# Kernel optimization log

Measured on AMD Instinct MI355X. Metric: run time of the kernel, lower is better.

The kernel has to match this reference:

```python
import jax, jax.numpy as jnp
import numpy as np

# hetero-graph meta: (relation, src_type, dst_type)
RELS = [("a2b", "a", "b"), ("b2a", "b", "a"), ("a2g", "a", "g"), ("g2a", "g", "a"),
        ("b2g", "b", "g"), ("g2b", "g", "b"), ("a2a", "a", "a"), ("b2b", "b", "b"), ("g2g", "g", "g")]
N = {"a": 100000, "b": 150000, "g": 2000}
E = {"a2b": 300000, "b2a": 300000, "a2g": 100000, "g2a": 100000,
     "b2g": 150000, "g2b": 150000, "a2a": 100000, "b2b": 150000, "g2g": 2000}
D = 128
N_LAYERS = 2
BN_EPS = 1e-5


def setup_inputs() -> dict:
    key = jax.random.key(0)
    ks = jax.random.split(key, 32)
    inp = {
        "feat_a": jax.random.normal(ks[0], (N["a"], D), jnp.float32),
        "feat_b": jax.random.normal(ks[1], (N["b"], D), jnp.float32),
        "feat_g": jax.random.normal(ks[2], (N["g"], D), jnp.float32),
        "W": jax.random.normal(ks[3], (N_LAYERS, 9, D, D), jnp.float32) * (1.0 / np.sqrt(D)),
        "bias": jnp.zeros((N_LAYERS, 9, D), jnp.float32),
        "gamma": jnp.ones((N_LAYERS, 9, D), jnp.float32),
        "beta": jnp.zeros((N_LAYERS, 9, D), jnp.float32),
    }
    i = 4
    for name, st, dt in RELS:
        inp[f"e_{name}_src"] = jax.random.randint(ks[i], (E[name],), 0, N[st], jnp.int32); i += 1
        inp[f"e_{name}_dst"] = jax.random.randint(ks[i], (E[name],), 0, N[dt], jnp.int32); i += 1
    return inp


def _gconv(x_src, src, dst, n_src, n_dst, W_r, b_r, g_r, be_r):
    """DGL GraphConv(norm='both') + (eval dropout = identity) + BatchNorm1d (batch stats)."""
    ones_e = jnp.ones(src.shape[0], x_src.dtype)
    out_deg = jax.ops.segment_sum(ones_e, src, num_segments=n_src)   # src out-degree
    in_deg = jax.ops.segment_sum(ones_e, dst, num_segments=n_dst)    # dst in-degree
    ns = jnp.where(out_deg > 0, jax.lax.rsqrt(jnp.maximum(out_deg, 1.0)), 0.0)
    nd = jnp.where(in_deg > 0, jax.lax.rsqrt(jnp.maximum(in_deg, 1.0)), 0.0)
    h = x_src * ns[:, None]                                           # [n_src, D]
    m = jax.ops.segment_sum(h[src], dst, num_segments=n_dst)         # gather-scatter over edges
    out = (m @ W_r) * nd[:, None] + b_r                               # [n_dst, D]
    mu = out.mean(axis=0)
    var = out.var(axis=0)                                             # biased var, as torch BN
    return (out - mu) * jax.lax.rsqrt(var + BN_EPS) * g_r + be_r


def _forward(feat_a, feat_b, feat_g, W, bias, gamma, beta, edges):
    feat = {"a": feat_a, "b": feat_b, "g": feat_g}
    resid = feat
    for l in range(N_LAYERS):
        acc = {"a": 0.0, "b": 0.0, "g": 0.0}
        for r, (name, st, dt) in enumerate(RELS):
            src, dst = edges[name]
            acc[dt] = acc[dt] + _gconv(feat[st], src, dst, N[st], N[dt],
                                       W[l, r], bias[l, r], gamma[l, r], beta[l, r])
        feat = acc  # HeteroGraphConv aggregate='sum'
    return (feat["a"] + resid["a"], feat["b"] + resid["b"], feat["g"] + resid["g"])


def reference(feat_a, feat_b, feat_g, W, bias, gamma, beta,
              e_a2b_src, e_a2b_dst, e_b2a_src, e_b2a_dst, e_a2g_src, e_a2g_dst,
              e_g2a_src, e_g2a_dst, e_b2g_src, e_b2g_dst, e_g2b_src, e_g2b_dst,
              e_a2a_src, e_a2a_dst, e_b2b_src, e_b2b_dst, e_g2g_src, e_g2g_dst):
    edges = {"a2b": (e_a2b_src, e_a2b_dst), "b2a": (e_b2a_src, e_b2a_dst),
             "a2g": (e_a2g_src, e_a2g_dst), "g2a": (e_g2a_src, e_g2a_dst),
             "b2g": (e_b2g_src, e_b2g_dst), "g2b": (e_g2b_src, e_g2b_dst),
             "a2a": (e_a2a_src, e_a2a_dst), "b2b": (e_b2b_src, e_b2b_dst),
             "g2g": (e_g2g_src, e_g2g_dst)}
    return _forward(feat_a, feat_b, feat_g, W, bias, gamma, beta, edges)
```

## Files before the change

kernel.cpp:

```cpp
#include <hip/hip_runtime.h>
#include <cstdint>

#define D 128

typedef __attribute__((ext_vector_type(8))) short short8;
typedef __attribute__((ext_vector_type(4))) float f32x4;

__device__ inline ushort f2bf(float f) {
    uint u = __float_as_uint(f);
    uint r = (u + 0x7fffu + ((u >> 16) & 1u)) >> 16;
    return (ushort)r;
}
__device__ inline float bf2f(ushort u) { return __uint_as_float(((uint)u) << 16); }


__global__ void k_count(const int* __restrict__ src, const int* __restrict__ dst,
                        int E, float* __restrict__ degs, float* __restrict__ degd) {
    int i = blockIdx.x * blockDim.x + threadIdx.x;
    if (i < E) {
        atomicAdd(&degs[src[i]], 1.0f);
        atomicAdd(&degd[dst[i]], 1.0f);
    }
}

__global__ void k_rsqrt(float* __restrict__ p, int n) {
    int i = blockIdx.x * blockDim.x + threadIdx.x;
    if (i < n) {
        float d = p[i];
        p[i] = d > 0.0f ? rsqrtf(d) : 0.0f;
    }
}

__global__ void k_scan1(const float* __restrict__ cnt, int* __restrict__ off,
                        int* __restrict__ bsum, int n) {
    __shared__ int s[256];
    int t = threadIdx.x, i = blockIdx.x * 256 + t;
    int v = (i < n) ? (int)cnt[i] : 0;
    int acc = v;
    s[t] = acc; __syncthreads();
    for (int d = 1; d < 256; d <<= 1) {
        int add = (t >= d) ? s[t - d] : 0;
        __syncthreads();
        acc += add; s[t] = acc; __syncthreads();
    }
    if (i < n) off[i] = acc - v;
    if (t == 255) bsum[blockIdx.x] = acc;
}

__global__ __launch_bounds__(1024) void k_scan2(int* __restrict__ bsum, int nb) {
    __shared__ int s[1024];
    int t = threadIdx.x;
    int i0 = t * 3;
    int v0 = (i0     < nb) ? bsum[i0]     : 0;
    int v1 = (i0 + 1 < nb) ? bsum[i0 + 1] : 0;
    int v2 = (i0 + 2 < nb) ? bsum[i0 + 2] : 0;
    int tot = v0 + v1 + v2;
    int acc = tot;
    s[t] = acc; __syncthreads();
    for (int d = 1; d < 1024; d <<= 1) {
        int add = (t >= d) ? s[t - d] : 0;
        __syncthreads();
        acc += add; s[t] = acc; __syncthreads();
    }
    int base = acc - tot;
    if (i0     < nb) bsum[i0]     = base;
    if (i0 + 1 < nb) bsum[i0 + 1] = base + v0;
    if (i0 + 2 < nb) bsum[i0 + 2] = base + v0 + v1;
}

__global__ void k_scan3(int* __restrict__ off, const int* __restrict__ bsum, int n) {
    int i = blockIdx.x * 256 + threadIdx.x;
    if (i < n) off[i] += bsum[blockIdx.x];
}

__global__ void k_fill(const int* __restrict__ src, const int* __restrict__ dst,
                       int E, int* __restrict__ offs, int* __restrict__ sorted) {
    int e = blockIdx.x * blockDim.x + threadIdx.x;
    if (e < E) {
        int pos = atomicAdd(&offs[dst[e]], 1);
        sorted[pos] = src[e];
    }
}

__global__ void k_prepw(const float* __restrict__ W, ushort* __restrict__ Wf) {
    int i = blockIdx.x * 256 + threadIdx.x;
    if (i < 18 * 16384) {
        int r = i >> 14, j = i & 16383;
        int e = j & 7, lane = (j >> 3) & 63, kbi = (j >> 9) & 3, c = j >> 11;
        int lm = lane & 15, lg = lane >> 4;
        int k = kbi * 32 + lg * 8 + e, ncol = c * 16 + lm;
        Wf[i] = f2bf(W[(r << 14) + (k << 7) + ncol]);
    }
}


__device__ inline float4 loadx(const float* x, size_t idx) { return *(const float4*)(x + idx); }
__device__ inline float4 loadx(const ushort* x, size_t idx) {
    ushort4 u = *(const ushort4*)(x + idx);
    float4 v;
    v.x = bf2f(u.x); v.y = bf2f(u.y); v.z = bf2f(u.z); v.w = bf2f(u.w);
    return v;
}

template <typename XT>
__global__ __launch_bounds__(256) void k_gather_row(
    const XT* __restrict__ x, const float* __restrict__ ns,
    const float* __restrict__ nd,
    const int* __restrict__ OFFS, int gdbase,
    const int* __restrict__ sorted, int n_dst,
    ushort* __restrict__ m) {
    __shared__ float4 part[8][32];
    int row = blockIdx.x;
    if (row >= n_dst) return;
    int t = threadIdx.x;
    int g = t >> 5, q = t & 31;
    int c4 = q * 4;
    int gd = gdbase + row;
    int beg = (gd == 0) ? 0 : OFFS[gd - 1];
    int end = OFFS[gd];
    float4 acc = {0.f, 0.f, 0.f, 0.f};
    for (int j = beg + g; j < end; j += 8) {
        int s = sorted[j];
        float w = ns[s];
        float4 v = loadx(x, ((size_t)s << 7) + c4);
        acc.x += v.x * w; acc.y += v.y * w; acc.z += v.z * w; acc.w += v.w * w;
    }
    part[g][q] = acc;
    __syncthreads();
    if (g == 0) {
        float4 a = part[0][q];
        #pragma unroll
        for (int gg = 1; gg < 8; ++gg) {
            float4 b = part[gg][q];
            a.x += b.x; a.y += b.y; a.z += b.z; a.w += b.w;
        }
        float sc = nd[row];
        ushort4 o;
        o.x = f2bf(a.x * sc); o.y = f2bf(a.y * sc);
        o.z = f2bf(a.z * sc); o.w = f2bf(a.w * sc);
        *(ushort4*)(m + ((size_t)row << 7) + c4) = o;
    }
}

__global__ __launch_bounds__(256) void k_gemm_mfma(
    const ushort* __restrict__ mb, const ushort* __restrict__ Wf,
    int n, float* __restrict__ outp, float* __restrict__ stats) {
    __shared__ ushort Wl[16384];
    __shared__ float Sl[256];
    int t = threadIdx.x;
    int w = t >> 6, lane = t & 63, lm = lane & 15, lg = lane >> 4;
    Sl[t] = 0.0f;

    #pragma unroll
    for (int i = 0; i < 8; ++i) {
        int ci = t + 256 * i;
        *(short8*)&Wl[ci * 8] = *(const short8*)&Wf[ci * 8];
    }
    __syncthreads();

    int R = (blockIdx.x * 4 + w) * 32;
    float rs1[8] = {0.f, 0.f, 0.f, 0.f, 0.f, 0.f, 0.f, 0.f};
    float rs2[8] = {0.f, 0.f, 0.f, 0.f, 0.f, 0.f, 0.f, 0.f};

    if (R < n) {
        f32x4 acc[2][8] = {};
        int r0 = R + lm, r1 = R + 16 + lm;
        const ushort* a0p = mb + (((size_t)r0) << 7) + lg * 8;
        const ushort* a1p = mb + (((size_t)r1) << 7) + lg * 8;
        bool v0 = r0 < n, v1 = r1 < n;
        #pragma unroll
        for (int kbi = 0; kbi < 4; ++kbi) {
            short8 a0 = {}, a1 = {};
            if (v0) a0 = *(const short8*)(a0p + kbi * 32);
            if (v1) a1 = *(const short8*)(a1p + kbi * 32);
            #pragma unroll
            for (int c = 0; c < 8; ++c) {
                short8 b = *(short8*)&Wl[((c * 4 + kbi) * 64 + lane) * 8];
                acc[0][c] = __builtin_amdgcn_mfma_f32_16x16x32_bf16(a0, b, acc[0][c], 0, 0, 0);
                acc[1][c] = __builtin_amdgcn_mfma_f32_16x16x32_bf16(a1, b, acc[1][c], 0, 0, 0);
            }
        }
        #pragma unroll
        for (int m = 0; m < 2; ++m) {
            int rowb = R + m * 16 + lg * 4;
            #pragma unroll
            for (int c = 0; c < 8; ++c) {
                f32x4 v = acc[m][c];
                rs1[c] += v[0] + v[1] + v[2] + v[3];
                rs2[c] += v[0] * v[0] + v[1] * v[1] + v[2] * v[2] + v[3] * v[3];
                #pragma unroll
                for (int i2 = 0; i2 < 4; ++i2) {
                    int row = rowb + i2;
                    if (row < n)
                        outp[((size_t)row << 7) + c * 16 + lm] = v[i2];
                }
            }
        }
    }

    #pragma unroll
    for (int c = 0; c < 8; ++c) {
        float s1 = rs1[c], s2 = rs2[c];
        s1 += __shfl_xor(s1, 16); s1 += __shfl_xor(s1, 32);
        s2 += __shfl_xor(s2, 16); s2 += __shfl_xor(s2, 32);
        if (lg == 0) {
            atomicAdd(&Sl[c * 16 + lm], s1);
            atomicAdd(&Sl[128 + c * 16 + lm], s2);
        }
    }
    __syncthreads();
    atomicAdd(&stats[t], Sl[t]);
}


template <typename XT>
__global__ __launch_bounds__(512) void k_fused2(
    const XT* __restrict__ x, const float* __restrict__ ns,
    const float* __restrict__ nd,
    const int* __restrict__ OFFS, int gdbase,
    const int* __restrict__ sorted,
    const ushort* __restrict__ Wf,
    int n, float* __restrict__ outp, float* __restrict__ stats) {
    __shared__ ushort Wl[16384];
    __shared__ float Sl[256];
    int t = threadIdx.x;
    if (t < 256) Sl[t] = 0.0f;

    #pragma unroll
    for (int i = 0; i < 4; ++i) {
        int ci = t + 512 * i;
        *(short8*)&Wl[ci * 8] = *(const short8*)&Wf[ci * 8];
    }

    int w = t >> 6, lane = t & 63, lm = lane & 15, lg = lane >> 4;
    int R = blockIdx.x * 128 + w * 16;
    int row = R + lm;

    float a[4][8] = {};
    float scale = 0.0f;
    if (row < n) {
        int gd = gdbase + row;
        int beg = (gd == 0) ? 0 : OFFS[gd - 1];
        int end = OFFS[gd];
        for (int j = beg; j < end; ++j) {
            int s = sorted[j];
            float wgt = ns[s];
            size_t xb = (size_t)s << 7;
            #pragma unroll
            for (int kbi = 0; kbi < 4; ++kbi) {
                int cb = (kbi * 4 + lg) * 8;
                float4 u0 = loadx(x, xb + cb);
                float4 u1 = loadx(x, xb + cb + 4);
                a[kbi][0] += u0.x * wgt; a[kbi][1] += u0.y * wgt;
                a[kbi][2] += u0.z * wgt; a[kbi][3] += u0.w * wgt;
                a[kbi][4] += u1.x * wgt; a[kbi][5] += u1.y * wgt;
                a[kbi][6] += u1.z * wgt; a[kbi][7] += u1.w * wgt;
            }
        }
        scale = nd[row];
    }

    short8 af[4];
    #pragma unroll
    for (int kbi = 0; kbi < 4; ++kbi) {
        #pragma unroll
        for (int e = 0; e < 8; ++e)
            af[kbi][e] = (short)f2bf(a[kbi][e] * scale);
    }

    __syncthreads();

    float rs1[8] = {0.f, 0.f, 0.f, 0.f, 0.f, 0.f, 0.f, 0.f};
    float rs2[8] = {0.f, 0.f, 0.f, 0.f, 0.f, 0.f, 0.f, 0.f};

    if (R < n) {
        f32x4 acc[8] = {};
        #pragma unroll
        for (int kbi = 0; kbi < 4; ++kbi) {
            #pragma unroll
            for (int c = 0; c < 8; ++c) {
                short8 b = *(short8*)&Wl[((c * 4 + kbi) * 64 + lane) * 8];
                acc[c] = __builtin_amdgcn_mfma_f32_16x16x32_bf16(af[kbi], b, acc[c], 0, 0, 0);
            }
        }
        int rowb = R + lg * 4;
        #pragma unroll
        for (int c = 0; c < 8; ++c) {
            f32x4 v = acc[c];
            rs1[c] += v[0] + v[1] + v[2] + v[3];
            rs2[c] += v[0] * v[0] + v[1] * v[1] + v[2] * v[2] + v[3] * v[3];
            #pragma unroll
            for (int i2 = 0; i2 < 4; ++i2) {
                int crow = rowb + i2;
                if (crow < n)
                    outp[((size_t)crow << 7) + c * 16 + lm] = v[i2];
            }
        }
    }

    #pragma unroll
    for (int c = 0; c < 8; ++c) {
        float s1 = rs1[c], s2 = rs2[c];
        s1 += __shfl_xor(s1, 16); s1 += __shfl_xor(s1, 32);
        s2 += __shfl_xor(s2, 16); s2 += __shfl_xor(s2, 32);
        if (lg == 0) {
            atomicAdd(&Sl[c * 16 + lm], s1);
            atomicAdd(&Sl[128 + c * 16 + lm], s2);
        }
    }
    __syncthreads();
    if (t < 256) atomicAdd(&stats[t], Sl[t]);
}


__global__ void k_norm3_bf(const float4* __restrict__ o0, const float4* __restrict__ o1,
                           const float4* __restrict__ o2,
                           const float* __restrict__ st0, const float* __restrict__ st1,
                           const float* __restrict__ st2,
                           const float* __restrict__ g0, const float* __restrict__ g1,
                           const float* __restrict__ g2,
                           const float* __restrict__ b0, const float* __restrict__ b1,
                           const float* __restrict__ b2,
                           float inv_n, int total4, ushort* __restrict__ dst) {
    __shared__ float sc[3][128], sh[3][128];
    int t = threadIdx.x;
    if (t < 128) {
        float mu0 = st0[t] * inv_n, va0 = st0[128 + t] * inv_n - mu0 * mu0;
        float s0 = g0[t] * rsqrtf(va0 + 1e-5f); sc[0][t] = s0; sh[0][t] = b0[t] - mu0 * s0;
        float mu1 = st1[t] * inv_n, va1 = st1[128 + t] * inv_n - mu1 * mu1;
        float s1 = g1[t] * rsqrtf(va1 + 1e-5f); sc[1][t] = s1; sh[1][t] = b1[t] - mu1 * s1;
        float mu2 = st2[t] * inv_n, va2 = st2[128 + t] * inv_n - mu2 * mu2;
        float s2 = g2[t] * rsqrtf(va2 + 1e-5f); sc[2][t] = s2; sh[2][t] = b2[t] - mu2 * s2;
    }
    __syncthreads();
    for (int i = blockIdx.x * blockDim.x + t; i < total4; i += gridDim.x * blockDim.x) {
        int c4 = (i & 31) * 4;
        float4 v0 = o0[i], v1 = o1[i], v2 = o2[i];
        float4 r;
        r.x = (v0.x * sc[0][c4+0] + sh[0][c4+0]) + (v1.x * sc[1][c4+0] + sh[1][c4+0]) + (v2.x * sc[2][c4+0] + sh[2][c4+0]);
        r.y = (v0.y * sc[0][c4+1] + sh[0][c4+1]) + (v1.y * sc[1][c4+1] + sh[1][c4+1]) + (v2.y * sc[2][c4+1] + sh[2][c4+1]);
        r.z = (v0.z * sc[0][c4+2] + sh[0][c4+2]) + (v1.z * sc[1][c4+2] + sh[1][c4+2]) + (v2.z * sc[2][c4+2] + sh[2][c4+2]);
        r.w = (v0.w * sc[0][c4+3] + sh[0][c4+3]) + (v1.w * sc[1][c4+3] + sh[1][c4+3]) + (v2.w * sc[2][c4+3] + sh[2][c4+3]);
        ushort4 o;
        o.x = f2bf(r.x); o.y = f2bf(r.y); o.z = f2bf(r.z); o.w = f2bf(r.w);
        *(ushort4*)(dst + (size_t)i * 4) = o;
    }
}

__global__ void k_norm3_f32(const float4* __restrict__ o0, const float4* __restrict__ o1,
                            const float4* __restrict__ o2,
                            const float* __restrict__ st0, const float* __restrict__ st1,
                            const float* __restrict__ st2,
                            const float* __restrict__ g0, const float* __restrict__ g1,
                            const float* __restrict__ g2,
                            const float* __restrict__ b0, const float* __restrict__ b1,
                            const float* __restrict__ b2,
                            float inv_n, int total4, float4* __restrict__ dst,
                            const float4* __restrict__ resid4) {
    __shared__ float sc[3][128], sh[3][128];
    int t = threadIdx.x;
    if (t < 128) {
        float mu0 = st0[t] * inv_n, va0 = st0[128 + t] * inv_n - mu0 * mu0;
        float s0 = g0[t] * rsqrtf(va0 + 1e-5f); sc[0][t] = s0; sh[0][t] = b0[t] - mu0 * s0;
        float mu1 = st1[t] * inv_n, va1 = st1[128 + t] * inv_n - mu1 * mu1;
        float s1 = g1[t] * rsqrtf(va1 + 1e-5f); sc[1][t] = s1; sh[1][t] = b1[t] - mu1 * s1;
        float mu2 = st2[t] * inv_n, va2 = st2[128 + t] * inv_n - mu2 * mu2;
        float s2 = g2[t] * rsqrtf(va2 + 1e-5f); sc[2][t] = s2; sh[2][t] = b2[t] - mu2 * s2;
    }
    __syncthreads();
    for (int i = blockIdx.x * blockDim.x + t; i < total4; i += gridDim.x * blockDim.x) {
        int c4 = (i & 31) * 4;
        float4 v0 = o0[i], v1 = o1[i], v2 = o2[i], d = resid4[i];
        float4 r;
        r.x = (v0.x * sc[0][c4+0] + sh[0][c4+0]) + (v1.x * sc[1][c4+0] + sh[1][c4+0]) + (v2.x * sc[2][c4+0] + sh[2][c4+0]) + d.x;
        r.y = (v0.y * sc[0][c4+1] + sh[0][c4+1]) + (v1.y * sc[1][c4+1] + sh[1][c4+1]) + (v2.y * sc[2][c4+1] + sh[2][c4+1]) + d.y;
        r.z = (v0.z * sc[0][c4+2] + sh[0][c4+2]) + (v1.z * sc[1][c4+2] + sh[1][c4+2]) + (v2.z * sc[2][c4+2] + sh[2][c4+2]) + d.z;
        r.w = (v0.w * sc[0][c4+3] + sh[0][c4+3]) + (v1.w * sc[1][c4+3] + sh[1][c4+3]) + (v2.w * sc[2][c4+3] + sh[2][c4+3]) + d.w;
        dst[i] = r;
    }
}


extern "C" void kernel_launch(void* const* d_in, const int* in_sizes, int n_in,
                              void* d_out, int out_size, void* d_ws, size_t ws_size,
                              hipStream_t stream) {
    static const int NT[3]   = {100000, 150000, 2000};
    static const int RE[9]   = {300000, 300000, 100000, 100000, 150000, 150000, 100000, 150000, 2000};
    static const int RSRC[9] = {0, 1, 0, 2, 1, 2, 0, 1, 2};
    static const int RDST[9] = {1, 0, 2, 0, 2, 1, 0, 1, 2};
    static const int DREL[3][3] = {{1, 3, 6}, {0, 5, 7}, {2, 4, 8}};
    const int TOT_N = 756000;
    const int NB = (TOT_N + 255) / 256;

    const float* feat_in[3] = {(const float*)d_in[0], (const float*)d_in[1], (const float*)d_in[2]};
    const float* W     = (const float*)d_in[3];
    const float* gamma = (const float*)d_in[5];
    const float* beta  = (const float*)d_in[6];
    float* ws  = (float*)d_ws;
    float* out = (float*)d_out;

    int ns_base[9], nd_base[9];
    {
        int s = 0, d = 0;
        for (int r = 0; r < 9; ++r) {
            ns_base[r] = s; s += NT[RSRC[r]];
            nd_base[r] = d; d += NT[RDST[r]];
        }
    }

    const size_t H_A    = 0;
    const size_t H_B    = H_A + 6400000;
    const size_t H_G    = H_B + 9600000;
    const size_t MBUF   = H_G + 128000;
    const size_t OUT    = MBUF + 9600000;
    const size_t WT     = OUT + 3 * 19200000;
    const size_t STATS  = WT + 147456;
    const size_t NS     = STATS + 4608;
    const size_t ND     = NS + 756000;
    const size_t OFFS   = ND + 756000;
    const size_t SORTED = OFFS + 756000;
    const size_t BSUM   = SORTED + 1352000;

    ushort* h_feat[3] = {(ushort*)(ws + H_A), (ushort*)(ws + H_B), (ushort*)(ws + H_G)};
    float* out_feat[3] = {out, out + 12800000, out + 32000000};
    ushort* mbuf   = (ushort*)(ws + MBUF);
    float*  obuf[3] = {ws + OUT, ws + OUT + 19200000, ws + OUT + 38400000};
    ushort* wt     = (ushort*)(ws + WT);
    float*  stats0 = ws + STATS;
    float*  ns_blk = ws + NS;
    float*  nd_blk = ws + ND;
    int*    offs   = (int*)(ws + OFFS);
    int*    sorted = (int*)(ws + SORTED);
    int*    bsum   = (int*)(ws + BSUM);

    hipMemsetAsync(ws + STATS, 0, (4608 + 2 * 756000) * sizeof(float), stream);

    for (int r = 0; r < 9; ++r) {
        const int* src = (const int*)d_in[7 + 2 * r];
        const int* dst = (const int*)d_in[8 + 2 * r];
        k_count<<<(RE[r] + 255) / 256, 256, 0, stream>>>(
            src, dst, RE[r], ns_blk + ns_base[r], nd_blk + nd_base[r]);
    }
    k_scan1<<<NB, 256, 0, stream>>>(nd_blk, offs, bsum, TOT_N);
    k_scan2<<<1, 1024, 0, stream>>>(bsum, NB);
    k_scan3<<<NB, 256, 0, stream>>>(offs, bsum, TOT_N);
    for (int r = 0; r < 9; ++r) {
        const int* src = (const int*)d_in[7 + 2 * r];
        const int* dst = (const int*)d_in[8 + 2 * r];
        k_fill<<<(RE[r] + 255) / 256, 256, 0, stream>>>(
            src, dst, RE[r], offs + nd_base[r], sorted);
    }
    k_rsqrt<<<(2 * TOT_N + 255) / 256, 256, 0, stream>>>(ns_blk, 2 * TOT_N);
    k_prepw<<<(18 * 16384 + 255) / 256, 256, 0, stream>>>(W, wt);

    for (int l = 0; l < 2; ++l) {
        for (int dt = 0; dt < 3; ++dt) {
            int n_dst = NT[dt];
            const int* rl = DREL[dt];

            for (int s = 0; s < 3; ++s) {
                int r = rl[s];
                int st = RSRC[r];
                float* stats = stats0 + (size_t)(l * 9 + r) * 256;
                const ushort* wfr = wt + (size_t)(l * 9 + r) * 16384;

                if (dt == 2) {
                    if (l == 0)
                        k_gather_row<float><<<n_dst, 256, 0, stream>>>(
                            feat_in[st], ns_blk + ns_base[r], nd_blk + nd_base[r],
                            offs, nd_base[r], sorted, n_dst, mbuf);
                    else
                        k_gather_row<ushort><<<n_dst, 256, 0, stream>>>(
                            h_feat[st], ns_blk + ns_base[r], nd_blk + nd_base[r],
                            offs, nd_base[r], sorted, n_dst, mbuf);
                    k_gemm_mfma<<<(n_dst + 127) / 128, 256, 0, stream>>>(
                        mbuf, wfr, n_dst, obuf[s], stats);
                } else {
                    int nblk = (n_dst + 127) / 128;
                    if (l == 0)
                        k_fused2<float><<<nblk, 512, 0, stream>>>(
                            feat_in[st], ns_blk + ns_base[r], nd_blk + nd_base[r],
                            offs, nd_base[r], sorted, wfr, n_dst, obuf[s], stats);
                    else
                        k_fused2<ushort><<<nblk, 512, 0, stream>>>(
                            h_feat[st], ns_blk + ns_base[r], nd_blk + nd_base[r],
                            offs, nd_base[r], sorted, wfr, n_dst, obuf[s], stats);
                }
            }

            int r0 = rl[0], r1 = rl[1], r2 = rl[2];
            const float* st0 = stats0 + (size_t)(l * 9 + r0) * 256;
            const float* st1 = stats0 + (size_t)(l * 9 + r1) * 256;
            const float* st2 = stats0 + (size_t)(l * 9 + r2) * 256;
            const float* g0 = gamma + (size_t)(l * 9 + r0) * D;
            const float* g1 = gamma + (size_t)(l * 9 + r1) * D;
            const float* g2 = gamma + (size_t)(l * 9 + r2) * D;
            const float* b0 = beta + (size_t)(l * 9 + r0) * D;
            const float* b1 = beta + (size_t)(l * 9 + r1) * D;
            const float* b2 = beta + (size_t)(l * 9 + r2) * D;
            int total4 = n_dst * 32;
            int ngrid = (total4 + 255) / 256;
            if (ngrid > 2048) ngrid = 2048;
            float inv_n = 1.0f / (float)n_dst;

            if (l == 0)
                k_norm3_bf<<<ngrid, 256, 0, stream>>>(
                    (const float4*)obuf[0], (const float4*)obuf[1], (const float4*)obuf[2],
                    st0, st1, st2, g0, g1, g2, b0, b1, b2,
                    inv_n, total4, h_feat[dt]);
            else
                k_norm3_f32<<<ngrid, 256, 0, stream>>>(
                    (const float4*)obuf[0], (const float4*)obuf[1], (const float4*)obuf[2],
                    st0, st1, st2, g0, g1, g2, b0, b1, b2,
                    inv_n, total4, (float4*)out_feat[dt], (const float4*)feat_in[dt]);
        }
    }
}
```

Measured before the change: 1.470 ms.

## Batch three relations per destination type into one fused launch, prefetch edge indices

Replaces the three per-relation k_fused2 launches for the a and b destination types with one k_fused3 launch. Each block picks its relation from blockIdx modulo 3, using a struct of per-relation pointers. This removes launch gaps and lets blocks from different relations run together to fill the GPU. It also software-prefetches the next sorted edge index in both the gather_row and fused loops, to shorten the dependent load chain. Interleaving the relations may reduce cache locality within each relation's source features.

```diff
diff --git a/kernel.cpp b/kernel.cpp
--- a/kernel.cpp
+++ b/kernel.cpp
@@ -119,11 +119,15 @@
     int beg = (gd == 0) ? 0 : OFFS[gd - 1];
     int end = OFFS[gd];
     float4 acc = {0.f, 0.f, 0.f, 0.f};
-    for (int j = beg + g; j < end; j += 8) {
-        int s = sorted[j];
+    int j = beg + g;
+    int sN = (j < end) ? sorted[j] : 0;
+    while (j < end) {
+        int s = sN;
+        if (j + 8 < end) sN = sorted[j + 8];
         float w = ns[s];
         float4 v = loadx(x, ((size_t)s << 7) + c4);
         acc.x += v.x * w; acc.y += v.y * w; acc.z += v.z * w; acc.w += v.w * w;
+        j += 8;
     }
     part[g][q] = acc;
     __syncthreads();
@@ -213,16 +217,32 @@
 }
 
 
+struct FatArgs {
+    const void*  x[3];
+    const float* ns[3];
+    const float* nd[3];
+    const ushort* wf[3];
+    float* outp[3];
+    float* stats[3];
+    int gdbase[3];
+};
+
 template <typename XT>
-__global__ __launch_bounds__(512) void k_fused2(
-    const XT* __restrict__ x, const float* __restrict__ ns,
-    const float* __restrict__ nd,
-    const int* __restrict__ OFFS, int gdbase,
-    const int* __restrict__ sorted,
-    const ushort* __restrict__ Wf,
-    int n, float* __restrict__ outp, float* __restrict__ stats) {
+__global__ __launch_bounds__(512) void k_fused3(
+    FatArgs fa, const int* __restrict__ OFFS, const int* __restrict__ sorted,
+    int n) {
     __shared__ ushort Wl[16384];
     __shared__ float Sl[256];
+    int rel  = blockIdx.x % 3;
+    int tile = blockIdx.x / 3;
+    const XT*    x     = (const XT*)fa.x[rel];
+    const float* ns    = fa.ns[rel];
+    const float* nd    = fa.nd[rel];
+    const ushort* Wf   = fa.wf[rel];
+    float* outp        = fa.outp[rel];
+    float* stats       = fa.stats[rel];
+    int gdbase         = fa.gdbase[rel];
+
     int t = threadIdx.x;
     if (t < 256) Sl[t] = 0.0f;
 
@@ -233,7 +253,7 @@
     }
 
     int w = t >> 6, lane = t & 63, lm = lane & 15, lg = lane >> 4;
-    int R = blockIdx.x * 128 + w * 16;
+    int R = tile * 128 + w * 16;
     int row = R + lm;
 
     float a[4][8] = {};
@@ -242,8 +262,11 @@
         int gd = gdbase + row;
         int beg = (gd == 0) ? 0 : OFFS[gd - 1];
         int end = OFFS[gd];
-        for (int j = beg; j < end; ++j) {
-            int s = sorted[j];
+        int j = beg;
+        int sN = (j < end) ? sorted[j] : 0;
+        while (j < end) {
+            int s = sN;
+            if (j + 1 < end) sN = sorted[j + 1];
             float wgt = ns[s];
             size_t xb = (size_t)s << 7;
             #pragma unroll
@@ -256,6 +279,7 @@
                 a[kbi][4] += u1.x * wgt; a[kbi][5] += u1.y * wgt;
                 a[kbi][6] += u1.z * wgt; a[kbi][7] += u1.w * wgt;
             }
+            ++j;
         }
         scale = nd[row];
     }
@@ -458,13 +482,12 @@
             int n_dst = NT[dt];
             const int* rl = DREL[dt];
 
-            for (int s = 0; s < 3; ++s) {
-                int r = rl[s];
-                int st = RSRC[r];
-                float* stats = stats0 + (size_t)(l * 9 + r) * 256;
-                const ushort* wfr = wt + (size_t)(l * 9 + r) * 16384;
-
-                if (dt == 2) {
+            if (dt == 2) {
+                for (int s = 0; s < 3; ++s) {
+                    int r = rl[s];
+                    int st = RSRC[r];
+                    float* stats = stats0 + (size_t)(l * 9 + r) * 256;
+                    const ushort* wfr = wt + (size_t)(l * 9 + r) * 16384;
                     if (l == 0)
                         k_gather_row<float><<<n_dst, 256, 0, stream>>>(
                             feat_in[st], ns_blk + ns_base[r], nd_blk + nd_base[r],
@@ -475,17 +498,25 @@
                             offs, nd_base[r], sorted, n_dst, mbuf);
                     k_gemm_mfma<<<(n_dst + 127) / 128, 256, 0, stream>>>(
                         mbuf, wfr, n_dst, obuf[s], stats);
-                } else {
-                    int nblk = (n_dst + 127) / 128;
-                    if (l == 0)
-                        k_fused2<float><<<nblk, 512, 0, stream>>>(
-                            feat_in[st], ns_blk + ns_base[r], nd_blk + nd_base[r],
-                            offs, nd_base[r], sorted, wfr, n_dst, obuf[s], stats);
-                    else
-                        k_fused2<ushort><<<nblk, 512, 0, stream>>>(
-                            h_feat[st], ns_blk + ns_base[r], nd_blk + nd_base[r],
-                            offs, nd_base[r], sorted, wfr, n_dst, obuf[s], stats);
                 }
+            } else {
+                FatArgs fa;
+                for (int s = 0; s < 3; ++s) {
+                    int r = rl[s];
+                    int st = RSRC[r];
+                    fa.x[s]      = (l == 0) ? (const void*)feat_in[st] : (const void*)h_feat[st];
+                    fa.ns[s]     = ns_blk + ns_base[r];
+                    fa.nd[s]     = nd_blk + nd_base[r];
+                    fa.wf[s]     = wt + (size_t)(l * 9 + r) * 16384;
+                    fa.outp[s]   = obuf[s];
+                    fa.stats[s]  = stats0 + (size_t)(l * 9 + r) * 256;
+                    fa.gdbase[s] = nd_base[r];
+                }
+                int nblk = (n_dst + 127) / 128;
+                if (l == 0)
+                    k_fused3<float><<<nblk * 3, 512, 0, stream>>>(fa, offs, sorted, n_dst);
+                else
+                    k_fused3<ushort><<<nblk * 3, 512, 0, stream>>>(fa, offs, sorted, n_dst);
             }
 
             int r0 = rl[0], r1 = rl[1], r2 = rl[2];
```

Result: faster. 1.257 ms (-14.5%).
